# Kernel optimization log

Hardware: AMD Instinct MI355X
Metric: run time of the kernel (lower is better)

The kernel has to match this reference:

```python
import jax, jax.numpy as jnp
import numpy as np

B, L, D = 2, 401, 128


def setup_inputs() -> dict:
    key = jax.random.key(0)
    ks = jax.random.split(key, 9)
    s = 1.0 / np.sqrt(D)
    return {
        "x": jax.random.normal(ks[0], (B, L, D), dtype=jnp.float32),
        # nn.Bilinear weight (out=D, in1=D, in2=D) and bias (D,)
        "W_bil": jax.random.uniform(ks[1], (D, D, D), jnp.float32, -s, s),
        "b_bil": jax.random.uniform(ks[2], (D,), jnp.float32, -s, s),
        # LayerNorm(D)
        "ln_g": jnp.ones((D,), jnp.float32),
        "ln_b": jnp.zeros((D,), jnp.float32),
        # Linear(D, D)
        "W1": jax.random.uniform(ks[3], (D, D), jnp.float32, -s, s),
        "b1": jax.random.uniform(ks[4], (D,), jnp.float32, -s, s),
        # Linear(D, 1)
        "w2": jax.random.uniform(ks[5], (D,), jnp.float32, -s, s),
        "b2": jax.random.uniform(ks[6], (1,), jnp.float32, -s, s),
    }


def reference(x, W_bil, b_bil, ln_g, ln_b, W1, b1, w2, b2):
    # Bilinear: pair[b,i,j,k] = x[b,i,:] @ W_bil[k] @ x[b,j,:] + b_bil[k]
    # Contract in two steps to avoid an O(L^2 D^2) intermediate:
    tmp = jnp.einsum('bid,kde->bike', x, W_bil)          # (B,L,D,D)
    pair = jnp.einsum('bike,bje->bijk', tmp, x) + b_bil  # (B,L,L,D)
    # LayerNorm over D
    mu = jnp.mean(pair, axis=-1, keepdims=True)
    var = jnp.mean(jnp.square(pair - mu), axis=-1, keepdims=True)
    h = (pair - mu) * jax.lax.rsqrt(var + 1e-5) * ln_g + ln_b
    # Linear -> GELU (exact, torch default) -> Dropout(eval: identity) -> Linear(D,1)
    h = jax.nn.gelu(jnp.einsum('bijd,ed->bije', h, W1) + b1, approximate=False)
    contact = jnp.einsum('bijd,d->bij', h, w2) + b2[0]   # (B,L,L)
    return 0.5 * (contact + jnp.swapaxes(contact, 1, 2))
```

## Files before the change

### kernel.cpp

```cpp
#include <hip/hip_runtime.h>
#include <hip/hip_bf16.h>

#define L 401
#define D 128
#define BATCH 2
#define PADU 136
#define PADB 272

typedef __attribute__((ext_vector_type(8))) short short8;
typedef __attribute__((ext_vector_type(4))) float f32x4;

__device__ __forceinline__ ushort bf16_bits(float f) {
  __hip_bfloat16 h = __float2bfloat16(f);
  return *reinterpret_cast<ushort*>(&h);
}

__device__ __forceinline__ float gelu_fast(float v) {
  const float a = fabsf(v) * 0.70710678118654752f;
  const float t = __builtin_amdgcn_rcpf(fmaf(a, 0.47047f, 1.0f));
  float p = fmaf(t, 0.3739278f, -0.0479399f);
  p = fmaf(p, t, 0.1740121f);
  p = p * t;
  const float e = __builtin_amdgcn_exp2f(a * a * -1.4426950408889634f);
  const float q = p * e;
  const float cdf = (v < 0.f) ? q : 1.0f - q;
  return v * cdf;
}

__device__ __forceinline__ short8 frag_read_swz(const char* lds, int row, int cb) {
  return *(const short8*)(lds + row * 256 + (cb ^ ((row & 7) << 4)));
}

__device__ __forceinline__ void stage_swz(char* lds, const __hip_bfloat16* src,
                                          int row0, int rowmax, int tid) {
#pragma unroll
  for (int it = 0; it < 4; ++it) {
    int r = it * 32 + (tid >> 4);
    int cb = (tid & 15) * 16;
    int sr = row0 + r;
    sr = sr > rowmax ? rowmax : sr;
    short8 v = *(const short8*)((const char*)src + (size_t)sr * 256 + cb);
    *(short8*)(lds + r * 256 + (cb ^ ((r & 7) << 4))) = v;
  }
}

__device__ __forceinline__ void stage_pad(char* lds, const __hip_bfloat16* src,
                                          int row0, int rowmax, int tid) {
#pragma unroll
  for (int it = 0; it < 4; ++it) {
    int r = it * 32 + (tid >> 4);
    int cb = (tid & 15) * 16;
    int sr = row0 + r;
    sr = sr > rowmax ? rowmax : sr;
    short8 v = *(const short8*)((const char*)src + (size_t)sr * 256 + cb);
    *(short8*)(lds + r * PADB + cb) = v;
  }
}

__global__ void prep_kernel(const float* __restrict__ x, const float* __restrict__ W_bil,
                            const float* __restrict__ W1, const float* __restrict__ ln_g,
                            const float* __restrict__ ln_b, const float* __restrict__ b1,
                            __hip_bfloat16* __restrict__ xbf, __hip_bfloat16* __restrict__ wbt,
                            __hip_bfloat16* __restrict__ wgbf, float* __restrict__ s1,
                            float* __restrict__ s2b1) {
  __shared__ alignas(16) ushort t[128 * PADU];
  __shared__ float red[8];
  const int bid = blockIdx.x;
  const int tid = threadIdx.x;
  if (bid < 128) {
    const float* in = W_bil + (size_t)bid * D * D;
#pragma unroll
    for (int it = 0; it < 16; ++it) {
      int idx = it * 256 + tid;
      int d = idx >> 5;
      int m = idx & 31;
      int e = m * 4;
      int swz = (m & 15) << 3;
      float4 f4 = ((const float4*)in)[idx];
      char* base = (char*)t;
      *(ushort*)(base + (size_t)(e + 0) * PADB + ((2 * d) ^ swz)) = bf16_bits(f4.x);
      *(ushort*)(base + (size_t)(e + 1) * PADB + ((2 * d) ^ swz)) = bf16_bits(f4.y);
      *(ushort*)(base + (size_t)(e + 2) * PADB + ((2 * d) ^ swz)) = bf16_bits(f4.z);
      *(ushort*)(base + (size_t)(e + 3) * PADB + ((2 * d) ^ swz)) = bf16_bits(f4.w);
    }
    __syncthreads();
    ushort* out = (ushort*)(wbt + (size_t)bid * D * D);
    const int e = tid >> 1;
    const int dh = (tid & 1) * 64;
    const int swz = ((e >> 2) & 15) << 3;
    const char* base = (const char*)t + (size_t)e * PADB;
#pragma unroll
    for (int c = 0; c < 16; ++c) {
      int d0 = dh + c * 4;
      unsigned long long v = *(const unsigned long long*)(base + ((2 * d0) ^ swz));
      *(unsigned long long*)&out[e * D + d0] = v;
    }
  } else if (bid < 154) {
    const int n4 = (BATCH * L * D) / 4;
    int i4 = (bid - 128) * 1024 + tid;
#pragma unroll
    for (int c = 0; c < 4; ++c) {
      int idx = i4 + c * 256;
      if (idx < n4) {
        float4 f4 = ((const float4*)x)[idx];
        ushort4 o;
        o.x = bf16_bits(f4.x); o.y = bf16_bits(f4.y);
        o.z = bf16_bits(f4.z); o.w = bf16_bits(f4.w);
        ((ushort4*)xbf)[idx] = o;
      }
    }
  } else {
    const int e = bid - 154;
    float s1p = 0.f, s2p = 0.f;
    if (tid < 128) {
      const int d = tid;
      const float wv = W1[e * D + d];
      const float wg = wv * ln_g[d];
      wgbf[e * D + d] = __float2bfloat16(wg);
      s1p = wg;
      s2p = wv * ln_b[d];
    }
#pragma unroll
    for (int m = 1; m <= 32; m <<= 1) {
      s1p += __shfl_xor(s1p, m);
      s2p += __shfl_xor(s2p, m);
    }
    const int wv_ = tid >> 6;
    if ((tid & 63) == 0) { red[wv_ * 2] = s1p; red[wv_ * 2 + 1] = s2p; }
    __syncthreads();
    if (tid == 0) {
      s1[e] = red[0] + red[2] + red[4] + red[6];
      s2b1[e] = red[1] + red[3] + red[5] + red[7] + b1[e];
    }
  }
}

__global__ __launch_bounds__(512, 4) void gemm_tmp(const __hip_bfloat16* __restrict__ xbf,
                                                   const __hip_bfloat16* __restrict__ wbt,
                                                   __hip_bfloat16* __restrict__ tmp) {
  __shared__ char ldsE[128 * 256];
  __shared__ char ldsI[128 * 256];
  const int tid = threadIdx.x;
  const int lane = tid & 63;
  const int w = tid >> 6;
  const int c0 = lane & 15;
  const int lg = lane >> 4;
  const int kt = blockIdx.x;
  const int i0 = blockIdx.y * 128;
  const int b = blockIdx.z;

  stage_swz(ldsI, xbf + (size_t)b * L * D, i0, L - 1, tid);
  stage_swz(ldsE, wbt + (size_t)kt * D * D, 0, 127, tid);
  __syncthreads();

  f32x4 acc[8];
#pragma unroll
  for (int cf = 0; cf < 8; ++cf) acc[cf] = (f32x4){0.f, 0.f, 0.f, 0.f};

#pragma unroll
  for (int ks = 0; ks < 4; ++ks) {
    const int cb = ks * 64 + lg * 16;
    short8 ae = frag_read_swz(ldsE, w * 16 + c0, cb);
#pragma unroll
    for (int cf = 0; cf < 8; ++cf) {
      short8 bi = frag_read_swz(ldsI, cf * 16 + c0, cb);
      acc[cf] = __builtin_amdgcn_mfma_f32_16x16x32_bf16(ae, bi, acc[cf], 0, 0, 0);
    }
  }

  ushort* outp = (ushort*)tmp;
  const int e0 = w * 16 + lg * 4;
#pragma unroll
  for (int cf = 0; cf < 8; ++cf) {
    const int i = i0 + cf * 16 + c0;
    if (i < L) {
      uint lo = (uint)bf16_bits(acc[cf][0]) | ((uint)bf16_bits(acc[cf][1]) << 16);
      uint hi = (uint)bf16_bits(acc[cf][2]) | ((uint)bf16_bits(acc[cf][3]) << 16);
      uint2 v; v.x = lo; v.y = hi;
      *(uint2*)(outp + ((size_t)(b * L + i)) * (D * D) + kt * D + e0) = v;
    }
  }
}

__global__ __launch_bounds__(512, 4) void fused_contact(
    const __hip_bfloat16* __restrict__ xbf, const __hip_bfloat16* __restrict__ tmp,
    const __hip_bfloat16* __restrict__ wgbf, const float* __restrict__ b_bil,
    const float* __restrict__ s1, const float* __restrict__ s2b1,
    const float* __restrict__ w2, const float* __restrict__ b2,
    float* __restrict__ cont) {
  __shared__ char ldsX[128 * PADB];
  __shared__ char ldsT[128 * PADB];
  const int tid = threadIdx.x;
  const int lane = tid & 63;
  const int w = tid >> 6;
  const int c0 = lane & 15;
  const int lg = lane >> 4;
  const int b = blockIdx.z;
  const int i = blockIdx.y;
  const int j0 = blockIdx.x * 128;
  const int jme = j0 + w * 16 + c0;
  const bool live = (j0 + w * 16) < L;

  stage_pad(ldsX, xbf + (size_t)b * L * D, j0, L - 1, tid);
  stage_pad(ldsT, tmp + ((size_t)(b * L + i)) * (D * D), 0, 127, tid);

  short8 wgreg[4];
  {
    const char* wsrc = (const char*)wgbf;
    const int cb = (tid & 15) * 16;
#pragma unroll
    for (int it = 0; it < 4; ++it) {
      int r = it * 32 + (tid >> 4);
      wgreg[it] = *(const short8*)(wsrc + (size_t)r * 256 + cb);
    }
  }
  __syncthreads();

  const int ownBase = (w * 16 + c0) * PADB;
  float rs = 0.f, nm = 0.f;

  if (live) {
    f32x4 acc1[8];
#pragma unroll
    for (int kf = 0; kf < 8; ++kf) acc1[kf] = (f32x4){0.f, 0.f, 0.f, 0.f};

#pragma unroll
    for (int ks = 0; ks < 4; ++ks) {
      short8 bx = *(const short8*)(ldsX + ownBase + lg * 16 + ks * 64);
#pragma unroll
      for (int kf = 0; kf < 8; ++kf) {
        short8 at = *(const short8*)(ldsT + (kf * 16 + c0) * PADB + lg * 16 + ks * 64);
        acc1[kf] = __builtin_amdgcn_mfma_f32_16x16x32_bf16(at, bx, acc1[kf], 0, 0, 0);
      }
    }

    float s = 0.f, q = 0.f;
#pragma unroll
    for (int kf = 0; kf < 8; ++kf) {
      const float4 bb = *(const float4*)&b_bil[kf * 16 + lg * 4];
      acc1[kf][0] += bb.x; acc1[kf][1] += bb.y;
      acc1[kf][2] += bb.z; acc1[kf][3] += bb.w;
#pragma unroll
      for (int r = 0; r < 4; ++r) {
        const float v = acc1[kf][r];
        s += v;
        q += v * v;
      }
    }
    s += __shfl_xor(s, 16); s += __shfl_xor(s, 32);
    q += __shfl_xor(q, 16); q += __shfl_xor(q, 32);
    const float m = s * (1.f / 128.f);
    const float var = q * (1.f / 128.f) - m * m;
    rs = __builtin_amdgcn_rsqf(var + 1e-5f);
    nm = -rs * m;

#pragma unroll
    for (int kf = 0; kf < 8; ++kf) {
      uint lo = (uint)bf16_bits(acc1[kf][0]) | ((uint)bf16_bits(acc1[kf][1]) << 16);
      uint hi = (uint)bf16_bits(acc1[kf][2]) | ((uint)bf16_bits(acc1[kf][3]) << 16);
      uint2 v; v.x = lo; v.y = hi;
      *(uint2*)(ldsX + ownBase + kf * 32 + lg * 8) = v;
    }
  }
  __syncthreads();

  {
    const int cb = (tid & 15) * 16;
#pragma unroll
    for (int it = 0; it < 4; ++it) {
      int r = it * 32 + (tid >> 4);
      *(short8*)(ldsT + r * PADB + cb) = wgreg[it];
    }
  }
  __syncthreads();
  if (!live) return;

  f32x4 acc2[8];
#pragma unroll
  for (int ef = 0; ef < 8; ++ef) acc2[ef] = (f32x4){0.f, 0.f, 0.f, 0.f};
#pragma unroll
  for (int ks = 0; ks < 4; ++ks) {
    short8 bx = *(const short8*)(ldsX + ownBase + lg * 16 + ks * 64);
#pragma unroll
    for (int ef = 0; ef < 8; ++ef) {
      short8 at = *(const short8*)(ldsT + (ef * 16 + c0) * PADB + lg * 16 + ks * 64);
      acc2[ef] = __builtin_amdgcn_mfma_f32_16x16x32_bf16(at, bx, acc2[ef], 0, 0, 0);
    }
  }

  float part = 0.f;
#pragma unroll
  for (int ef = 0; ef < 8; ++ef) {
    const int e0 = ef * 16 + lg * 4;
    const float4 s1v = *(const float4*)&s1[e0];
    const float4 c2v = *(const float4*)&s2b1[e0];
    const float4 w2v = *(const float4*)&w2[e0];
    const float v0 = fmaf(acc2[ef][0], rs, fmaf(nm, s1v.x, c2v.x));
    const float v1 = fmaf(acc2[ef][1], rs, fmaf(nm, s1v.y, c2v.y));
    const float v2 = fmaf(acc2[ef][2], rs, fmaf(nm, s1v.z, c2v.z));
    const float v3 = fmaf(acc2[ef][3], rs, fmaf(nm, s1v.w, c2v.w));
    part += gelu_fast(v0) * w2v.x;
    part += gelu_fast(v1) * w2v.y;
    part += gelu_fast(v2) * w2v.z;
    part += gelu_fast(v3) * w2v.w;
  }
  part += __shfl_xor(part, 16);
  part += __shfl_xor(part, 32);
  if (lg == 0 && jme < L) {
    cont[((size_t)(b * L + i)) * L + jme] = part + b2[0];
  }
}

__global__ void sym_kernel(const float* __restrict__ c, float* __restrict__ out) {
  int idx = blockIdx.x * 256 + threadIdx.x;
  const int n = BATCH * L * L;
  if (idx >= n) return;
  int b = idx / (L * L);
  int r = idx - b * (L * L);
  int i = r / L;
  int j = r - i * L;
  out[idx] = 0.5f * (c[(size_t)b * L * L + (size_t)i * L + j] +
                     c[(size_t)b * L * L + (size_t)j * L + i]);
}

extern "C" void kernel_launch(void* const* d_in, const int* in_sizes, int n_in,
                              void* d_out, int out_size, void* d_ws, size_t ws_size,
                              hipStream_t stream) {
  const float* x     = (const float*)d_in[0];
  const float* W_bil = (const float*)d_in[1];
  const float* b_bil = (const float*)d_in[2];
  const float* ln_g  = (const float*)d_in[3];
  const float* ln_b  = (const float*)d_in[4];
  const float* W1    = (const float*)d_in[5];
  const float* b1    = (const float*)d_in[6];
  const float* w2    = (const float*)d_in[7];
  const float* b2    = (const float*)d_in[8];
  float* out = (float*)d_out;

  char* ws = (char*)d_ws;
  __hip_bfloat16* xbf  = (__hip_bfloat16*)(ws + 0);
  __hip_bfloat16* wgbf = (__hip_bfloat16*)(ws + 205312);
  float* s1            = (float*)(ws + 238080);
  float* s2b1          = (float*)(ws + 238592);
  __hip_bfloat16* wbt  = (__hip_bfloat16*)(ws + 239104);
  __hip_bfloat16* tmp  = (__hip_bfloat16*)(ws + 4433408);
  float* cont          = (float*)(ws + 30713344);

  prep_kernel<<<282, 256, 0, stream>>>(x, W_bil, W1, ln_g, ln_b, b1,
                                       xbf, wbt, wgbf, s1, s2b1);
  gemm_tmp<<<dim3(D, 4, BATCH), 512, 0, stream>>>(xbf, wbt, tmp);
  fused_contact<<<dim3(4, L, BATCH), 512, 0, stream>>>(xbf, tmp, wgbf, b_bil,
                                                       s1, s2b1, w2, b2, cont);
  sym_kernel<<<(BATCH * L * L + 255) / 256, 256, 0, stream>>>(cont, out);
}
```

Measured before the change: 167.5 us.

## Load MFMA operands directly from global memory to halve LDS footprint

```diff
diff --git a/kernel.cpp b/kernel.cpp
--- a/kernel.cpp
+++ b/kernel.cpp
@@ -41,19 +41,6 @@
     sr = sr > rowmax ? rowmax : sr;
     short8 v = *(const short8*)((const char*)src + (size_t)sr * 256 + cb);
     *(short8*)(lds + r * 256 + (cb ^ ((r & 7) << 4))) = v;
-  }
-}
-
-__device__ __forceinline__ void stage_pad(char* lds, const __hip_bfloat16* src,
-                                          int row0, int rowmax, int tid) {
-#pragma unroll
-  for (int it = 0; it < 4; ++it) {
-    int r = it * 32 + (tid >> 4);
-    int cb = (tid & 15) * 16;
-    int sr = row0 + r;
-    sr = sr > rowmax ? rowmax : sr;
-    short8 v = *(const short8*)((const char*)src + (size_t)sr * 256 + cb);
-    *(short8*)(lds + r * PADB + cb) = v;
   }
 }
 
@@ -135,11 +122,10 @@
   }
 }
 
-__global__ __launch_bounds__(512, 4) void gemm_tmp(const __hip_bfloat16* __restrict__ xbf,
+__global__ __launch_bounds__(512, 6) void gemm_tmp(const __hip_bfloat16* __restrict__ xbf,
                                                    const __hip_bfloat16* __restrict__ wbt,
                                                    __hip_bfloat16* __restrict__ tmp) {
   __shared__ char ldsE[128 * 256];
-  __shared__ char ldsI[128 * 256];
   const int tid = threadIdx.x;
   const int lane = tid & 63;
   const int w = tid >> 6;
@@ -149,8 +135,16 @@
   const int i0 = blockIdx.y * 128;
   const int b = blockIdx.z;
 
-  stage_swz(ldsI, xbf + (size_t)b * L * D, i0, L - 1, tid);
   stage_swz(ldsE, wbt + (size_t)kt * D * D, 0, 127, tid);
+
+  const char* xbase = (const char*)(xbf + (size_t)b * L * D);
+  const char* xrows[8];
+#pragma unroll
+  for (int cf = 0; cf < 8; ++cf) {
+    int irow = i0 + cf * 16 + c0;
+    irow = irow < L ? irow : (L - 1);
+    xrows[cf] = xbase + (size_t)irow * 256;
+  }
   __syncthreads();
 
   f32x4 acc[8];
@@ -163,7 +157,7 @@
     short8 ae = frag_read_swz(ldsE, w * 16 + c0, cb);
 #pragma unroll
     for (int cf = 0; cf < 8; ++cf) {
-      short8 bi = frag_read_swz(ldsI, cf * 16 + c0, cb);
+      short8 bi = *(const short8*)(xrows[cf] + lg * 16 + ks * 64);
       acc[cf] = __builtin_amdgcn_mfma_f32_16x16x32_bf16(ae, bi, acc[cf], 0, 0, 0);
     }
   }
@@ -182,13 +176,12 @@
   }
 }
 
-__global__ __launch_bounds__(512, 4) void fused_contact(
+__global__ __launch_bounds__(512, 6) void fused_contact(
     const __hip_bfloat16* __restrict__ xbf, const __hip_bfloat16* __restrict__ tmp,
     const __hip_bfloat16* __restrict__ wgbf, const float* __restrict__ b_bil,
     const float* __restrict__ s1, const float* __restrict__ s2b1,
     const float* __restrict__ w2, const float* __restrict__ b2,
     float* __restrict__ cont) {
-  __shared__ char ldsX[128 * PADB];
   __shared__ char ldsT[128 * PADB];
   const int tid = threadIdx.x;
   const int lane = tid & 63;
@@ -199,41 +192,39 @@
   const int i = blockIdx.y;
   const int j0 = blockIdx.x * 128;
   const int jme = j0 + w * 16 + c0;
+  const int jclamp = jme < L ? jme : (L - 1);
   const bool live = (j0 + w * 16) < L;
 
-  stage_pad(ldsX, xbf + (size_t)b * L * D, j0, L - 1, tid);
-  stage_pad(ldsT, tmp + ((size_t)(b * L + i)) * (D * D), 0, 127, tid);
-
-  short8 wgreg[4];
   {
-    const char* wsrc = (const char*)wgbf;
-    const int cb = (tid & 15) * 16;
+    const char* tsrc = (const char*)(tmp + ((size_t)(b * L + i)) * (D * D));
 #pragma unroll
     for (int it = 0; it < 4; ++it) {
       int r = it * 32 + (tid >> 4);
-      wgreg[it] = *(const short8*)(wsrc + (size_t)r * 256 + cb);
-    }
-  }
+      int cb = (tid & 15) * 16;
+      short8 v = *(const short8*)(tsrc + (size_t)r * 256 + cb);
+      *(short8*)(ldsT + r * PADB + cb) = v;
+    }
+  }
+  const char* xrow = (const char*)(xbf + ((size_t)b * L + jclamp) * D);
+  short8 bxv[4];
+#pragma unroll
+  for (int ks = 0; ks < 4; ++ks) bxv[ks] = *(const short8*)(xrow + lg * 16 + ks * 64);
   __syncthreads();
 
-  const int ownBase = (w * 16 + c0) * PADB;
   float rs = 0.f, nm = 0.f;
-
+  f32x4 acc1[8];
   if (live) {
-    f32x4 acc1[8];
 #pragma unroll
     for (int kf = 0; kf < 8; ++kf) acc1[kf] = (f32x4){0.f, 0.f, 0.f, 0.f};
-
 #pragma unroll
     for (int ks = 0; ks < 4; ++ks) {
-      short8 bx = *(const short8*)(ldsX + ownBase + lg * 16 + ks * 64);
+      const int co = lg * 16 + ks * 64;
 #pragma unroll
       for (int kf = 0; kf < 8; ++kf) {
-        short8 at = *(const short8*)(ldsT + (kf * 16 + c0) * PADB + lg * 16 + ks * 64);
-        acc1[kf] = __builtin_amdgcn_mfma_f32_16x16x32_bf16(at, bx, acc1[kf], 0, 0, 0);
+        short8 at = *(const short8*)(ldsT + (kf * 16 + c0) * PADB + co);
+        acc1[kf] = __builtin_amdgcn_mfma_f32_16x16x32_bf16(at, bxv[ks], acc1[kf], 0, 0, 0);
       }
     }
-
     float s = 0.f, q = 0.f;
 #pragma unroll
     for (int kf = 0; kf < 8; ++kf) {
@@ -253,38 +244,33 @@
     const float var = q * (1.f / 128.f) - m * m;
     rs = __builtin_amdgcn_rsqf(var + 1e-5f);
     nm = -rs * m;
-
+  }
+  __syncthreads();
+  if (!live) return;
+
+  {
+    char* prow = ldsT + (w * 16 + c0) * PADB + lg * 8;
 #pragma unroll
     for (int kf = 0; kf < 8; ++kf) {
       uint lo = (uint)bf16_bits(acc1[kf][0]) | ((uint)bf16_bits(acc1[kf][1]) << 16);
       uint hi = (uint)bf16_bits(acc1[kf][2]) | ((uint)bf16_bits(acc1[kf][3]) << 16);
       uint2 v; v.x = lo; v.y = hi;
-      *(uint2*)(ldsX + ownBase + kf * 32 + lg * 8) = v;
-    }
-  }
-  __syncthreads();
-
-  {
-    const int cb = (tid & 15) * 16;
-#pragma unroll
-    for (int it = 0; it < 4; ++it) {
-      int r = it * 32 + (tid >> 4);
-      *(short8*)(ldsT + r * PADB + cb) = wgreg[it];
-    }
-  }
-  __syncthreads();
-  if (!live) return;
+      *(uint2*)(prow + kf * 32) = v;
+    }
+  }
 
   f32x4 acc2[8];
 #pragma unroll
   for (int ef = 0; ef < 8; ++ef) acc2[ef] = (f32x4){0.f, 0.f, 0.f, 0.f};
+  const char* wgc = (const char*)wgbf;
 #pragma unroll
   for (int ks = 0; ks < 4; ++ks) {
-    short8 bx = *(const short8*)(ldsX + ownBase + lg * 16 + ks * 64);
+    const int co = lg * 16 + ks * 64;
+    short8 bx2 = *(const short8*)(ldsT + (w * 16 + c0) * PADB + co);
 #pragma unroll
     for (int ef = 0; ef < 8; ++ef) {
-      short8 at = *(const short8*)(ldsT + (ef * 16 + c0) * PADB + lg * 16 + ks * 64);
-      acc2[ef] = __builtin_amdgcn_mfma_f32_16x16x32_bf16(at, bx, acc2[ef], 0, 0, 0);
+      short8 at = *(const short8*)(wgc + (size_t)(ef * 16 + c0) * 256 + co);
+      acc2[ef] = __builtin_amdgcn_mfma_f32_16x16x32_bf16(at, bx2, acc2[ef], 0, 0, 0);
     }
   }
 
```

Result: slower. 271.8 us (+62.3%).
